# Kernel optimization log

Measured on AMD Instinct MI355X. Metric: run time of the kernel, lower is better.

The kernel has to match this reference:

```python
import jax, jax.numpy as jnp
import numpy as np

B, S, D = 2, 2048, 1024
H, KV, HD = 16, 4, 64
E, TOPK, F = 8, 2, 2048
EPS = 1e-5
THETA = 10000.0


def setup_inputs() -> dict:
    key = jax.random.key(0)
    ks = jax.random.split(key, 12)
    sc = 0.02
    x = jax.random.normal(ks[0], (B, S, D), jnp.float32)
    # real RoPE tables
    inv = 1.0 / (THETA ** (np.arange(0, HD, 2, dtype=np.float32) / HD))
    t = np.arange(S, dtype=np.float32)
    f = np.outer(t, inv)  # [S, HD/2]
    freqs_cos = jnp.asarray(np.cos(f), jnp.float32)
    freqs_sin = jnp.asarray(np.sin(f), jnp.float32)
    return {
        "x": x,
        "freqs_cos": freqs_cos,
        "freqs_sin": freqs_sin,
        "attn_norm_w": jnp.ones((D,), jnp.float32),
        "ffn_norm_w": jnp.ones((D,), jnp.float32),
        "wq": jax.random.normal(ks[1], (D, H * HD), jnp.float32) * sc,
        "wk": jax.random.normal(ks[2], (D, KV * HD), jnp.float32) * sc,
        "wv": jax.random.normal(ks[3], (D, KV * HD), jnp.float32) * sc,
        "wo": jax.random.normal(ks[4], (H * HD, D), jnp.float32) * sc,
        "gate_w": jax.random.normal(ks[5], (D, E), jnp.float32) * sc,
        "w1": jax.random.normal(ks[6], (E, D, F), jnp.float32) * sc,
        "w2": jax.random.normal(ks[7], (E, F, D), jnp.float32) * sc,
        "w3": jax.random.normal(ks[8], (E, D, F), jnp.float32) * sc,
    }


def rmsnorm(x, w):
    return x * jax.lax.rsqrt(jnp.mean(x * x, axis=-1, keepdims=True) + EPS) * w


def apply_rope(xq, cos, sin):
    # xq: [B,S,h,HD]; cos/sin: [S, HD/2]
    xr, xi = xq[..., 0::2], xq[..., 1::2]
    c = cos[None, :, None, :]
    s = sin[None, :, None, :]
    out = jnp.stack([xr * c - xi * s, xr * s + xi * c], axis=-1)
    return out.reshape(xq.shape)


def attention(xn, freqs_cos, freqs_sin, wq, wk, wv, wo):
    q = (xn @ wq).reshape(B, S, H, HD)
    k = (xn @ wk).reshape(B, S, KV, HD)
    v = (xn @ wv).reshape(B, S, KV, HD)
    q = apply_rope(q, freqs_cos, freqs_sin)
    k = apply_rope(k, freqs_cos, freqs_sin)
    n_rep = H // KV
    k = jnp.repeat(k, n_rep, axis=2)  # [B,S,H,HD]
    v = jnp.repeat(v, n_rep, axis=2)
    scores = jnp.einsum("bqhd,bkhd->bhqk", q, k) / jnp.sqrt(jnp.float32(HD))
    causal = jnp.tril(jnp.ones((S, S), bool))
    scores = jnp.where(causal[None, None], scores, jnp.finfo(scores.dtype).min)
    probs = jax.nn.softmax(scores, axis=-1)
    out = jnp.einsum("bhqk,bkhd->bqhd", probs, v).reshape(B, S, H * HD)
    return out @ wo


def sparse_moe(hn, gate_w, w1, w2, w3):
    xf = hn.reshape(-1, D)  # [T, D]
    probs = jax.nn.softmax(xf @ gate_w, axis=-1)  # [T, E]
    topv, topi = jax.lax.top_k(probs, TOPK)
    topv = topv / jnp.sum(topv, axis=-1, keepdims=True)
    # dense [T, E] routing weights (0 for non-selected experts)
    wdense = jnp.sum(jax.nn.one_hot(topi, E, dtype=xf.dtype) * topv[..., None], axis=1)
    h1 = jax.nn.silu(jnp.einsum("td,edf->etf", xf, w1))
    h3 = jnp.einsum("td,edf->etf", xf, w3)
    y = jnp.einsum("etf,efd->etd", h1 * h3, w2)
    out = jnp.einsum("te,etd->td", wdense, y)
    return out.reshape(B, S, D)


def reference(x, freqs_cos, freqs_sin, attn_norm_w, ffn_norm_w,
              wq, wk, wv, wo, gate_w, w1, w2, w3):
    h = x + attention(rmsnorm(x, attn_norm_w), freqs_cos, freqs_sin, wq, wk, wv, wo)
    out = h + sparse_moe(rmsnorm(h, ffn_norm_w), gate_w, w1, w2, w3)
    return out
```

## Files before the change

kernel.cpp:

```cpp
#include <hip/hip_runtime.h>
#include <stdint.h>

typedef unsigned short u16;
typedef unsigned int u32;
typedef __attribute__((ext_vector_type(8))) short short8;
typedef __attribute__((ext_vector_type(8))) u16 us8;
typedef __attribute__((ext_vector_type(4))) u16 us4;
typedef __attribute__((ext_vector_type(4))) float f32x4;

constexpr int NB = 2;
constexpr int SEQ = 2048;
constexpr int DIM = 1024;
constexpr int NH = 16;
constexpr int HD = 64;
constexpr int NE = 8;
constexpr int FF = 2048;
constexpr int TOK = NB * SEQ;
constexpr int NQKV = 1536;
constexpr int NPAIR = TOK * 2;
constexpr float REPS = 1e-5f;

__device__ __forceinline__ u16 f2bf(float x) {
  union { float f; u32 u; } v; v.f = x;
  u32 r = v.u + 0x7fffu + ((v.u >> 16) & 1u);
  return (u16)(r >> 16);
}
__device__ __forceinline__ float bf2f(u16 h) {
  union { u32 u; float f; } v; v.u = ((u32)h) << 16;
  return v.f;
}

template <bool SPLIT>
__global__ __launch_bounds__(256) void tcvt_k(const float* __restrict__ src,
                                              u16* __restrict__ dhi,
                                              u16* __restrict__ dlo,
                                              int K, int N) {
  int z = blockIdx.z;
  src += (size_t)z * K * N;
  dhi += (size_t)z * K * N;
  if (SPLIT) dlo += (size_t)z * K * N;
  int n0 = blockIdx.x * 64, k0 = blockIdx.y * 64;
  __shared__ float tile[64][65];
  int t = threadIdx.x;
  int kk = t >> 4, nn4 = (t & 15) * 4;
#pragma unroll
  for (int i = 0; i < 4; i++) {
    int k = kk + i * 16;
    const float* p = src + (size_t)(k0 + k) * N + n0 + nn4;
    float4 v = *(const float4*)p;
    tile[nn4 + 0][k] = v.x;
    tile[nn4 + 1][k] = v.y;
    tile[nn4 + 2][k] = v.z;
    tile[nn4 + 3][k] = v.w;
  }
  __syncthreads();
  int nn = t >> 4, k4 = (t & 15) * 4;
#pragma unroll
  for (int i = 0; i < 4; i++) {
    int n = nn + i * 16;
    us4 hi, lo;
#pragma unroll
    for (int j = 0; j < 4; j++) {
      float f = tile[n][k4 + j];
      u16 h = f2bf(f);
      hi[j] = h;
      if (SPLIT) lo[j] = f2bf(f - bf2f(h));
    }
    *(us4*)(dhi + (size_t)(n0 + n) * K + k0 + k4) = hi;
    if (SPLIT) *(us4*)(dlo + (size_t)(n0 + n) * K + k0 + k4) = lo;
  }
}

template <bool SPLIT>
__global__ __launch_bounds__(256) void rmsnorm_k(const float* __restrict__ x,
                                                 const float* __restrict__ w,
                                                 u16* __restrict__ ohi,
                                                 u16* __restrict__ olo) {
  int row = blockIdx.x, t = threadIdx.x;
  float4 v = *(const float4*)(x + (size_t)row * DIM + t * 4);
  float ss = v.x * v.x + v.y * v.y + v.z * v.z + v.w * v.w;
#pragma unroll
  for (int m = 1; m < 64; m <<= 1) ss += __shfl_xor(ss, m);
  __shared__ float red[4];
  if ((t & 63) == 0) red[t >> 6] = ss;
  __syncthreads();
  float rstd = rsqrtf((red[0] + red[1] + red[2] + red[3]) * (1.0f / DIM) + REPS);
  float4 wv = *(const float4*)(w + t * 4);
  float os[4] = {v.x * rstd * wv.x, v.y * rstd * wv.y, v.z * rstd * wv.z,
                 v.w * rstd * wv.w};
  us4 hi, lo;
#pragma unroll
  for (int j = 0; j < 4; j++) {
    u16 h = f2bf(os[j]);
    hi[j] = h;
    if (SPLIT) lo[j] = f2bf(os[j] - bf2f(h));
  }
  *(us4*)(ohi + (size_t)row * DIM + t * 4) = hi;
  if (SPLIT) *(us4*)(olo + (size_t)row * DIM + t * 4) = lo;
}

template <int EPI, bool SPLIT, bool GATHER, bool DUAL>
__global__ __launch_bounds__(256) void gemm_k(
    const u16* __restrict__ Ah, const u16* __restrict__ Al,
    const u16* __restrict__ Bh, const u16* __restrict__ Bl,
    const u16* __restrict__ B1, int M, int N, int K, int ldc,
    float* __restrict__ Cf, u16* __restrict__ Cb, float* __restrict__ C2,
    const float* __restrict__ resid, const int* __restrict__ cnt,
    const int* __restrict__ pids, const float* __restrict__ pw) {
  constexpr int BN = SPLIT ? 64 : 128;
  constexpr int WCOL = BN / 2;
  constexpr int FN = BN / 32;

  int z = blockIdx.z;
  {
    size_t boff = (size_t)z * N * K;
    Bh += boff;
    if (SPLIT) Bl += boff;
    if (DUAL) B1 += boff;
  }
  int m0 = blockIdx.y * 128, n0 = blockIdx.x * BN;
  int tid = threadIdx.x, lane = tid & 63, wid = tid >> 6;
  int wm = wid >> 1, wn = wid & 1;

  __shared__ u16 sAh[128 * 64];
  __shared__ u16 sAl[SPLIT ? 128 * 64 : 8];
  __shared__ u16 sBh[BN * 64];
  __shared__ u16 sBl[SPLIT ? BN * 64 : 8];
  __shared__ u16 sB1[DUAL ? BN * 64 : 8];
  __shared__ int spid[GATHER ? 128 : 8];
  __shared__ int srow[GATHER ? 128 : 8];

  int cntz = M;
  if (GATHER) {
    cntz = cnt[z];
    if (m0 >= cntz) return;
    if (tid < 128) {
      int i = m0 + tid;
      if (i > cntz - 1) i = cntz - 1;
      int p = pids[z * NPAIR + i];
      spid[tid] = p;
      srow[tid] = (EPI == 2) ? (p >> 1) : p;
    }
  }
  __syncthreads();

  f32x4 zv = {0.f, 0.f, 0.f, 0.f};
  f32x4 acc[4][FN];
  f32x4 acc1[4][FN];
#pragma unroll
  for (int a = 0; a < 4; a++)
#pragma unroll
    for (int b = 0; b < FN; b++) {
      acc[a][b] = zv;
      acc1[a][b] = zv;
    }

  for (int k0 = 0; k0 < K; k0 += 64) {
    __syncthreads();
#pragma unroll
    for (int i = 0; i < 4; i++) {
      int cid = tid + i * 256;
      int r = cid >> 3, c = cid & 7;
      int sw = r * 64 + ((c ^ (r & 7)) * 8);
      size_t ar = GATHER ? (size_t)srow[r] : (size_t)(m0 + r);
      *(us8*)&sAh[sw] = *(const us8*)(Ah + ar * K + k0 + c * 8);
      if (SPLIT) *(us8*)&sAl[sw] = *(const us8*)(Al + ar * K + k0 + c * 8);
    }
#pragma unroll
    for (int i = 0; i < FN; i++) {
      int cid = tid + i * 256;
      int r = cid >> 3, c = cid & 7;
      int sw = r * 64 + ((c ^ (r & 7)) * 8);
      size_t br = (size_t)(n0 + r) * K + k0 + c * 8;
      *(us8*)&sBh[sw] = *(const us8*)(Bh + br);
      if (SPLIT) *(us8*)&sBl[sw] = *(const us8*)(Bl + br);
      if (DUAL) *(us8*)&sB1[sw] = *(const us8*)(B1 + br);
    }
    __syncthreads();
#pragma unroll
    for (int kc = 0; kc < 2; kc++) {
      int rr = lane & 15;
      int sw = (((kc * 4 + (lane >> 4)) ^ (rr & 7)) * 8);
      short8 a_h[4], a_l[4], b_h[FN], b_l[FN], b1f[FN];
#pragma unroll
      for (int f = 0; f < 4; f++) {
        int ra = wm * 64 + f * 16 + rr;
        a_h[f] = *(const short8*)&sAh[ra * 64 + sw];
        if (SPLIT) a_l[f] = *(const short8*)&sAl[ra * 64 + sw];
      }
#pragma unroll
      for (int f = 0; f < FN; f++) {
        int rb = wn * WCOL + f * 16 + rr;
        b_h[f] = *(const short8*)&sBh[rb * 64 + sw];
        if (SPLIT) b_l[f] = *(const short8*)&sBl[rb * 64 + sw];
        if (DUAL) b1f[f] = *(const short8*)&sB1[rb * 64 + sw];
      }
#pragma unroll
      for (int fm = 0; fm < 4; fm++)
#pragma unroll
        for (int fn = 0; fn < FN; fn++) {
          acc[fm][fn] = __builtin_amdgcn_mfma_f32_16x16x32_bf16(
              a_h[fm], b_h[fn], acc[fm][fn], 0, 0, 0);
          if (SPLIT) {
            acc[fm][fn] = __builtin_amdgcn_mfma_f32_16x16x32_bf16(
                a_h[fm], b_l[fn], acc[fm][fn], 0, 0, 0);
            acc[fm][fn] = __builtin_amdgcn_mfma_f32_16x16x32_bf16(
                a_l[fm], b_h[fn], acc[fm][fn], 0, 0, 0);
          }
          if (DUAL)
            acc1[fm][fn] = __builtin_amdgcn_mfma_f32_16x16x32_bf16(
                a_h[fm], b1f[fn], acc1[fm][fn], 0, 0, 0);
        }
    }
  }

#pragma unroll
  for (int fm = 0; fm < 4; fm++)
#pragma unroll
    for (int fn = 0; fn < FN; fn++)
#pragma unroll
      for (int rg = 0; rg < 4; rg++) {
        int rl = wm * 64 + fm * 16 + (lane >> 4) * 4 + rg;
        int col = n0 + wn * WCOL + fn * 16 + (lane & 15);
        float v = acc[fm][fn][rg];
        if (EPI == 0) {
          Cf[(size_t)(m0 + rl) * ldc + col] = v;
        } else if (EPI == 1) {
          size_t idx = (size_t)(m0 + rl) * ldc + col;
          float r2 = v + resid[idx];
          Cf[idx] = r2;
          C2[idx] = r2;
        } else if (EPI == 2) {
          if (m0 + rl < cntz) {
            float g = v / (1.0f + __expf(-v));
            float o = g * acc1[fm][fn][rg];
            Cb[(size_t)spid[rl] * ldc + col] = f2bf(o);
          }
        } else {
          if (m0 + rl < cntz) {
            int p = spid[rl];
            atomicAdd(&Cf[(size_t)(p >> 1) * ldc + col], pw[p] * v);
          }
        }
      }
}

__global__ __launch_bounds__(256) void rope_k(float* __restrict__ qkv,
                                              const float* __restrict__ fc,
                                              const float* __restrict__ fs) {
  int idx = blockIdx.x * 256 + threadIdx.x;
  int i = idx & 31;
  int hh = (idx >> 5) % 20;
  int t = idx / 640;
  if (t >= TOK) return;
  int s = t & (SEQ - 1);
  int base = (hh < 16) ? (hh * 64) : (1024 + (hh - 16) * 64);
  float c = fc[s * 32 + i], sn = fs[s * 32 + i];
  float* p = qkv + (size_t)t * NQKV + base + 2 * i;
  float xr = p[0], xi = p[1];
  p[0] = xr * c - xi * sn;
  p[1] = xr * sn + xi * c;
}

__global__ __launch_bounds__(256) void cvtkv_k(const float* __restrict__ qkv,
                                               u16* __restrict__ Kh,
                                               u16* __restrict__ Kl,
                                               u16* __restrict__ Vh,
                                               u16* __restrict__ Vl) {
  int kvt = blockIdx.x;
  int kvh = blockIdx.y;
  int b = blockIdx.z;
  int t = threadIdx.x;
  __shared__ float vt[64][65];
  size_t tile = ((size_t)((b * 4 + kvh) * 32 + kvt)) * 4096;
  int r = t >> 2, c4 = t & 3;
  {
    const float* kp = qkv + ((size_t)(b * SEQ + kvt * 64 + r)) * NQKV + 1024 +
                      kvh * 64 + c4 * 16;
    float ff[16];
#pragma unroll
    for (int q = 0; q < 4; q++) {
      float4 f = *(const float4*)(kp + q * 4);
      ff[q * 4 + 0] = f.x; ff[q * 4 + 1] = f.y;
      ff[q * 4 + 2] = f.z; ff[q * 4 + 3] = f.w;
    }
#pragma unroll
    for (int half = 0; half < 2; half++) {
      int c = c4 * 2 + half;
      us8 hi, lo;
#pragma unroll
      for (int j = 0; j < 8; j++) {
        float f = ff[half * 8 + j];
        u16 h = f2bf(f);
        hi[j] = h;
        lo[j] = f2bf(f - bf2f(h));
      }
      int off = r * 64 + ((c ^ (r & 7)) * 8);
      *(us8*)(Kh + tile + off) = hi;
      *(us8*)(Kl + tile + off) = lo;
    }
  }
  {
    const float* vp = qkv + ((size_t)(b * SEQ + kvt * 64 + r)) * NQKV + 1280 +
                      kvh * 64 + c4 * 16;
#pragma unroll
    for (int q = 0; q < 4; q++) {
      float4 f = *(const float4*)(vp + q * 4);
      vt[r][c4 * 16 + q * 4 + 0] = f.x;
      vt[r][c4 * 16 + q * 4 + 1] = f.y;
      vt[r][c4 * 16 + q * 4 + 2] = f.z;
      vt[r][c4 * 16 + q * 4 + 3] = f.w;
    }
  }
  __syncthreads();
  {
    int d = t >> 2, g4 = t & 3;
    float ff[16];
#pragma unroll
    for (int j = 0; j < 16; j++) ff[j] = vt[g4 * 16 + j][d];
#pragma unroll
    for (int half = 0; half < 2; half++) {
      int c = g4 * 2 + half;
      us8 hi, lo;
#pragma unroll
      for (int j = 0; j < 8; j++) {
        float f = ff[half * 8 + j];
        u16 h = f2bf(f);
        hi[j] = h;
        lo[j] = f2bf(f - bf2f(h));
      }
      int off = d * 64 + ((c ^ (d & 7)) * 8);
      *(us8*)(Vh + tile + off) = hi;
      *(us8*)(Vl + tile + off) = lo;
    }
  }
}

__global__ __launch_bounds__(256, 2) void flash_k(
    const float* __restrict__ qkv, const u16* __restrict__ Kg,
    const u16* __restrict__ Klg, const u16* __restrict__ Vg,
    const u16* __restrict__ Vlg, u16* __restrict__ ah, u16* __restrict__ al) {
  int pi = blockIdx.x;
  int h = blockIdx.y;
  int b = blockIdx.z;
  int qt[2] = {31 - pi, pi};
  int kvh = h >> 2;
  int tid = threadIdx.x, lane = tid & 63, wid = tid >> 6;
  int rr = lane & 15, g = lane >> 4;

  __shared__ u16 sKh[4096], sKl[4096], sVh[4096], sVl[4096];
  __shared__ u32 sP[4][1024];

  f32x4 zv = {0.f, 0.f, 0.f, 0.f};
  short8 aqh[2][2], aql[2][2];
#pragma unroll
  for (int u = 0; u < 2; u++) {
    int qrow = qt[u] * 64 + wid * 16 + rr;
    const float* qp =
        qkv + ((size_t)(b * SEQ + qrow)) * NQKV + h * 64 + g * 8;
#pragma unroll
    for (int kc = 0; kc < 2; kc++) {
      float4 f0 = *(const float4*)(qp + kc * 32);
      float4 f1 = *(const float4*)(qp + kc * 32 + 4);
      float ff[8] = {f0.x, f0.y, f0.z, f0.w, f1.x, f1.y, f1.z, f1.w};
#pragma unroll
      for (int j = 0; j < 8; j++) {
        u16 hi = f2bf(ff[j]);
        aqh[u][kc][j] = (short)hi;
        aql[u][kc][j] = (short)f2bf(ff[j] - bf2f(hi));
      }
    }
  }

  f32x4 o[2][4];
  float m_r[2][4], l_r[2][4];
#pragma unroll
  for (int u = 0; u < 2; u++)
#pragma unroll
    for (int i = 0; i < 4; i++) {
      o[u][i] = zv;
      m_r[u][i] = -3.0e38f;
      l_r[u][i] = 0.f;
    }

  size_t tb = ((size_t)(b * 4 + kvh) * 32) * 4096;
  int so = tid * 16;
  us8 rKh[2], rKl[2], rVh[2], rVl[2];
  {
    size_t go = tb + so;
    rKh[0] = *(const us8*)(Kg + go);  rKh[1] = *(const us8*)(Kg + go + 8);
    rKl[0] = *(const us8*)(Klg + go); rKl[1] = *(const us8*)(Klg + go + 8);
    rVh[0] = *(const us8*)(Vg + go);  rVh[1] = *(const us8*)(Vg + go + 8);
    rVl[0] = *(const us8*)(Vlg + go); rVl[1] = *(const us8*)(Vlg + go + 8);
  }

  int nt = qt[0];
  for (int kvt = 0; kvt <= nt; kvt++) {
    __syncthreads();
    *(us8*)&sKh[so] = rKh[0]; *(us8*)&sKh[so + 8] = rKh[1];
    *(us8*)&sKl[so] = rKl[0]; *(us8*)&sKl[so + 8] = rKl[1];
    *(us8*)&sVh[so] = rVh[0]; *(us8*)&sVh[so + 8] = rVh[1];
    *(us8*)&sVl[so] = rVl[0]; *(us8*)&sVl[so + 8] = rVl[1];
    if (kvt < nt) {
      size_t go = tb + (size_t)(kvt + 1) * 4096 + so;
      rKh[0] = *(const us8*)(Kg + go);  rKh[1] = *(const us8*)(Kg + go + 8);
      rKl[0] = *(const us8*)(Klg + go); rKl[1] = *(const us8*)(Klg + go + 8);
      rVh[0] = *(const us8*)(Vg + go);  rVh[1] = *(const us8*)(Vg + go + 8);
      rVl[0] = *(const us8*)(Vlg + go); rVl[1] = *(const us8*)(Vlg + go + 8);
    }
    __syncthreads();

#pragma unroll
    for (int u = 0; u < 2; u++) {
      if (!(u == 1 && kvt > qt[1])) {
        float pv[4][4];
#pragma unroll
        for (int c16 = 0; c16 < 4; c16++) {
          int rk = c16 * 16 + rr;
          f32x4 sacc = zv;
#pragma unroll
          for (int kc = 0; kc < 2; kc++) {
            int sw = rk * 64 + (((kc * 4 + g) ^ (rk & 7)) * 8);
            short8 bh = *(const short8*)&sKh[sw];
            short8 bl = *(const short8*)&sKl[sw];
            sacc = __builtin_amdgcn_mfma_f32_16x16x32_bf16(aqh[u][kc], bh,
                                                           sacc, 0, 0, 0);
            sacc = __builtin_amdgcn_mfma_f32_16x16x32_bf16(aqh[u][kc], bl,
                                                           sacc, 0, 0, 0);
            sacc = __builtin_amdgcn_mfma_f32_16x16x32_bf16(aql[u][kc], bh,
                                                           sacc, 0, 0, 0);
          }
          bool diag = (kvt == qt[u]);
#pragma unroll
          for (int rg = 0; rg < 4; rg++) {
            float val = sacc[rg] * 0.125f;
            if (diag) {
              int kv_l = c16 * 16 + rr;
              int q_l = wid * 16 + g * 4 + rg;
              if (kv_l > q_l) val = -3.0e38f;
            }
            pv[c16][rg] = val;
          }
        }
        float pm[4];
#pragma unroll
        for (int rg = 0; rg < 4; rg++)
          pm[rg] = fmaxf(fmaxf(pv[0][rg], pv[1][rg]),
                         fmaxf(pv[2][rg], pv[3][rg]));
#pragma unroll
        for (int m = 1; m < 16; m <<= 1)
#pragma unroll
          for (int rg = 0; rg < 4; rg++)
            pm[rg] = fmaxf(pm[rg], __shfl_xor(pm[rg], m));
        float scl[4];
#pragma unroll
        for (int rg = 0; rg < 4; rg++) {
          float mn = fmaxf(m_r[u][rg], pm[rg]);
          scl[rg] = __expf(m_r[u][rg] - mn);
          m_r[u][rg] = mn;
        }
#pragma unroll
        for (int c16 = 0; c16 < 4; c16++)
#pragma unroll
          for (int rg = 0; rg < 4; rg++)
            pv[c16][rg] = __expf(pv[c16][rg] - m_r[u][rg]);
        float rsum[4];
#pragma unroll
        for (int rg = 0; rg < 4; rg++)
          rsum[rg] = pv[0][rg] + pv[1][rg] + pv[2][rg] + pv[3][rg];
#pragma unroll
        for (int m = 1; m < 16; m <<= 1)
#pragma unroll
          for (int rg = 0; rg < 4; rg++) rsum[rg] += __shfl_xor(rsum[rg], m);
#pragma unroll
        for (int rg = 0; rg < 4; rg++)
          l_r[u][rg] = l_r[u][rg] * scl[rg] + rsum[rg];
#pragma unroll
        for (int d16 = 0; d16 < 4; d16++)
#pragma unroll
          for (int rg = 0; rg < 4; rg++) o[u][d16][rg] *= scl[rg];

#pragma unroll
        for (int c16 = 0; c16 < 4; c16++)
#pragma unroll
          for (int rg = 0; rg < 4; rg++) {
            int ql = g * 4 + rg;
            int kvl = c16 * 16 + rr;
            u16 hi = f2bf(pv[c16][rg]);
            u16 lo = f2bf(pv[c16][rg] - bf2f(hi));
            sP[wid][ql * 64 + (kvl ^ (((ql >> 2) & 3) << 4))] =
                ((u32)lo << 16) | (u32)hi;
          }
        short8 pah[2], pal[2];
#pragma unroll
        for (int kc = 0; kc < 2; kc++) {
          int xb = (kc * 32 + g * 8) ^ (((rr >> 2) & 3) << 4);
          const u32* pp = &sP[wid][rr * 64 + xb];
#pragma unroll
          for (int j = 0; j < 8; j++) {
            u32 w = pp[j];
            pah[kc][j] = (short)(w & 0xffffu);
            pal[kc][j] = (short)(w >> 16);
          }
        }
#pragma unroll
        for (int d16 = 0; d16 < 4; d16++) {
          int rv = d16 * 16 + rr;
#pragma unroll
          for (int kc = 0; kc < 2; kc++) {
            int sw = rv * 64 + (((kc * 4 + g) ^ (rv & 7)) * 8);
            short8 vh = *(const short8*)&sVh[sw];
            short8 vl = *(const short8*)&sVl[sw];
            o[u][d16] = __builtin_amdgcn_mfma_f32_16x16x32_bf16(
                pah[kc], vh, o[u][d16], 0, 0, 0);
            o[u][d16] = __builtin_amdgcn_mfma_f32_16x16x32_bf16(
                pah[kc], vl, o[u][d16], 0, 0, 0);
            o[u][d16] = __builtin_amdgcn_mfma_f32_16x16x32_bf16(
                pal[kc], vh, o[u][d16], 0, 0, 0);
          }
        }
      }
    }
  }

#pragma unroll
  for (int u = 0; u < 2; u++)
#pragma unroll
    for (int rg = 0; rg < 4; rg++) {
      float inv = 1.0f / l_r[u][rg];
      int qr = qt[u] * 64 + wid * 16 + g * 4 + rg;
      size_t obase = (size_t)(b * SEQ + qr) * 1024 + h * 64;
#pragma unroll
      for (int d16 = 0; d16 < 4; d16++) {
        float v = o[u][d16][rg] * inv;
        u16 hi = f2bf(v);
        ah[obase + d16 * 16 + rr] = hi;
        al[obase + d16 * 16 + rr] = f2bf(v - bf2f(hi));
      }
    }
}

__global__ __launch_bounds__(256) void route_k(const float* __restrict__ h,
                                               const float* __restrict__ wffn,
                                               const float* __restrict__ gw,
                                               int* __restrict__ cnt,
                                               int* __restrict__ pids,
                                               float* __restrict__ pw) {
  int t = blockIdx.x, tid = threadIdx.x;
  float4 v = *(const float4*)(h + (size_t)t * DIM + tid * 4);
  float ss = v.x * v.x + v.y * v.y + v.z * v.z + v.w * v.w;
#pragma unroll
  for (int m = 1; m < 64; m <<= 1) ss += __shfl_xor(ss, m);
  __shared__ float red[4];
  if ((tid & 63) == 0) red[tid >> 6] = ss;
  __syncthreads();
  float rstd = rsqrtf((red[0] + red[1] + red[2] + red[3]) * (1.0f / DIM) + REPS);
  float4 wv = *(const float4*)(wffn + tid * 4);
  float xn[4] = {v.x * rstd * wv.x, v.y * rstd * wv.y, v.z * rstd * wv.z,
                 v.w * rstd * wv.w};
  float pl[8] = {0, 0, 0, 0, 0, 0, 0, 0};
#pragma unroll
  for (int j = 0; j < 4; j++) {
    const float* gp = gw + (size_t)(tid * 4 + j) * 8;
    float4 g0 = *(const float4*)gp;
    float4 g1 = *(const float4*)(gp + 4);
    pl[0] += xn[j] * g0.x; pl[1] += xn[j] * g0.y;
    pl[2] += xn[j] * g0.z; pl[3] += xn[j] * g0.w;
    pl[4] += xn[j] * g1.x; pl[5] += xn[j] * g1.y;
    pl[6] += xn[j] * g1.z; pl[7] += xn[j] * g1.w;
  }
#pragma unroll
  for (int e = 0; e < 8; e++)
#pragma unroll
    for (int m = 1; m < 64; m <<= 1) pl[e] += __shfl_xor(pl[e], m);
  __shared__ float lred[4][8];
  if ((tid & 63) == 0)
#pragma unroll
    for (int e = 0; e < 8; e++) lred[tid >> 6][e] = pl[e];
  __syncthreads();
  if (tid == 0) {
    float lg[8];
#pragma unroll
    for (int e = 0; e < 8; e++)
      lg[e] = lred[0][e] + lred[1][e] + lred[2][e] + lred[3][e];
    int e1 = 0;
    float l1 = lg[0];
#pragma unroll
    for (int e = 1; e < 8; e++)
      if (lg[e] > l1) { l1 = lg[e]; e1 = e; }
    int e2 = -1;
    float l2 = -3.0e38f;
#pragma unroll
    for (int e = 0; e < 8; e++)
      if (e != e1 && lg[e] > l2) { l2 = lg[e]; e2 = e; }
    float w1 = 1.0f / (1.0f + expf(l2 - l1));
    float w2 = 1.0f / (1.0f + expf(l1 - l2));
    int p0 = atomicAdd(&cnt[e1], 1);
    pids[e1 * NPAIR + p0] = t * 2;
    pw[t * 2] = w1;
    int p1 = atomicAdd(&cnt[e2], 1);
    pids[e2 * NPAIR + p1] = t * 2 + 1;
    pw[t * 2 + 1] = w2;
  }
}

__global__ void zero_k(int* cnt) {
  if (threadIdx.x < 8) cnt[threadIdx.x] = 0;
}

extern "C" void kernel_launch(void* const* d_in, const int* in_sizes, int n_in,
                              void* d_out, int out_size, void* d_ws,
                              size_t ws_size, hipStream_t stream) {
  (void)in_sizes; (void)n_in; (void)out_size; (void)ws_size;
  const float* x = (const float*)d_in[0];
  const float* fc = (const float*)d_in[1];
  const float* fs = (const float*)d_in[2];
  const float* anw = (const float*)d_in[3];
  const float* fnw = (const float*)d_in[4];
  const float* wq = (const float*)d_in[5];
  const float* wk = (const float*)d_in[6];
  const float* wv = (const float*)d_in[7];
  const float* wo = (const float*)d_in[8];
  const float* gw = (const float*)d_in[9];
  const float* w1 = (const float*)d_in[10];
  const float* w2 = (const float*)d_in[11];
  const float* w3 = (const float*)d_in[12];
  float* outf = (float*)d_out;

  char* ws = (char*)d_ws;
  size_t off = 0;
  auto alloc = [&](size_t bytes) {
    void* p = ws + off;
    off += (bytes + 255) & ~(size_t)255;
    return p;
  };
  u16* wqkvT_h = (u16*)alloc((size_t)NQKV * DIM * 2);
  u16* wqkvT_l = (u16*)alloc((size_t)NQKV * DIM * 2);
  u16* woT_h = (u16*)alloc((size_t)DIM * DIM * 2);
  u16* woT_l = (u16*)alloc((size_t)DIM * DIM * 2);
  u16* w1T = (u16*)alloc((size_t)NE * FF * DIM * 2);
  u16* w3T = (u16*)alloc((size_t)NE * FF * DIM * 2);
  u16* w2T = (u16*)alloc((size_t)NE * DIM * FF * 2);
  u16* xnh = (u16*)alloc((size_t)TOK * DIM * 2);
  u16* xnl = (u16*)alloc((size_t)TOK * DIM * 2);
  float* qkvf = (float*)alloc((size_t)TOK * NQKV * 4);
  u16* attnh = (u16*)alloc((size_t)TOK * DIM * 2);
  u16* attnl = (u16*)alloc((size_t)TOK * DIM * 2);
  float* hbuf = (float*)alloc((size_t)TOK * DIM * 4);
  u16* hn = (u16*)alloc((size_t)TOK * DIM * 2);
  u16* h13 = (u16*)alloc((size_t)NPAIR * FF * 2);
  int* cnt = (int*)alloc(32);
  int* pids = (int*)alloc((size_t)NE * NPAIR * 4);
  float* pwbuf = (float*)alloc((size_t)NPAIR * 4);
  u16* Ksw_h = (u16*)alloc((size_t)NB * 4 * SEQ * 64 * 2);
  u16* Ksw_l = (u16*)alloc((size_t)NB * 4 * SEQ * 64 * 2);
  u16* Vsw_h = (u16*)alloc((size_t)NB * 4 * SEQ * 64 * 2);
  u16* Vsw_l = (u16*)alloc((size_t)NB * 4 * SEQ * 64 * 2);

  dim3 blk(256);
  hipLaunchKernelGGL((tcvt_k<true>), dim3(16, 16, 1), blk, 0, stream, wq,
                     wqkvT_h, wqkvT_l, 1024, 1024);
  hipLaunchKernelGGL((tcvt_k<true>), dim3(4, 16, 1), blk, 0, stream, wk,
                     wqkvT_h + 1024 * 1024, wqkvT_l + 1024 * 1024, 1024, 256);
  hipLaunchKernelGGL((tcvt_k<true>), dim3(4, 16, 1), blk, 0, stream, wv,
                     wqkvT_h + 1280 * 1024, wqkvT_l + 1280 * 1024, 1024, 256);
  hipLaunchKernelGGL((tcvt_k<true>), dim3(16, 16, 1), blk, 0, stream, wo, woT_h,
                     woT_l, 1024, 1024);
  hipLaunchKernelGGL((tcvt_k<false>), dim3(32, 16, 8), blk, 0, stream, w1, w1T,
                     (u16*)nullptr, 1024, 2048);
  hipLaunchKernelGGL((tcvt_k<false>), dim3(32, 16, 8), blk, 0, stream, w3, w3T,
                     (u16*)nullptr, 1024, 2048);
  hipLaunchKernelGGL((tcvt_k<false>), dim3(16, 32, 8), blk, 0, stream, w2, w2T,
                     (u16*)nullptr, 2048, 1024);
  hipLaunchKernelGGL((rmsnorm_k<true>), dim3(TOK), blk, 0, stream, x, anw, xnh,
                     xnl);
  hipLaunchKernelGGL((gemm_k<0, true, false, false>),
                     dim3(NQKV / 64, TOK / 128, 1), blk, 0, stream, xnh, xnl,
                     wqkvT_h, wqkvT_l, (const u16*)nullptr, TOK, NQKV, DIM,
                     NQKV, qkvf, (u16*)nullptr, (float*)nullptr,
                     (const float*)nullptr, (const int*)nullptr,
                     (const int*)nullptr, (const float*)nullptr);
  hipLaunchKernelGGL(rope_k, dim3((TOK * 20 * 32) / 256), blk, 0, stream, qkvf,
                     fc, fs);
  hipLaunchKernelGGL(cvtkv_k, dim3(SEQ / 64, 4, NB), blk, 0, stream, qkvf,
                     Ksw_h, Ksw_l, Vsw_h, Vsw_l);
  hipLaunchKernelGGL(flash_k, dim3(16, NH, NB), blk, 0, stream, qkvf, Ksw_h,
                     Ksw_l, Vsw_h, Vsw_l, attnh, attnl);
  hipLaunchKernelGGL((gemm_k<1, true, false, false>),
                     dim3(DIM / 64, TOK / 128, 1), blk, 0, stream, attnh, attnl,
                     woT_h, woT_l, (const u16*)nullptr, TOK, DIM, DIM, DIM,
                     hbuf, (u16*)nullptr, outf, x, (const int*)nullptr,
                     (const int*)nullptr, (const float*)nullptr);
  hipLaunchKernelGGL((rmsnorm_k<false>), dim3(TOK), blk, 0, stream, hbuf, fnw,
                     hn, (u16*)nullptr);
  hipLaunchKernelGGL(zero_k, dim3(1), dim3(64), 0, stream, cnt);
  hipLaunchKernelGGL(route_k, dim3(TOK), blk, 0, stream, hbuf, fnw, gw, cnt,
                     pids, pwbuf);
  hipLaunchKernelGGL((gemm_k<2, false, true, true>),
                     dim3(FF / 128, NPAIR / 128, NE), blk, 0, stream, hn,
                     (const u16*)nullptr, w1T, (const u16*)nullptr, w3T, NPAIR,
                     FF, DIM, FF, (float*)nullptr, h13, (float*)nullptr,
                     (const float*)nullptr, cnt, pids, pwbuf);
  hipLaunchKernelGGL((gemm_k<3, false, true, false>),
                     dim3(DIM / 128, NPAIR / 128, NE), blk, 0, stream, h13,
                     (const u16*)nullptr, w2T, (const u16*)nullptr,
                     (const u16*)nullptr, NPAIR, DIM, FF, DIM, outf,
                     (u16*)nullptr, (float*)nullptr, (const float*)nullptr, cnt,
                     pids, pwbuf);
}
```

Baseline: 651.0 us.

## Pipeline GEMM with triple-buffered direct-to-LDS loads and persistent MoE scheduling

```diff
diff --git a/kernel.cpp b/kernel.cpp
--- a/kernel.cpp
+++ b/kernel.cpp
@@ -20,6 +20,9 @@
 constexpr int NPAIR = TOK * 2;
 constexpr float REPS = 1e-5f;
 
+#define VMCNT(n) asm volatile("s_waitcnt vmcnt(" #n ")" ::: "memory")
+#define LGKM0 asm volatile("s_waitcnt lgkmcnt(0)" ::: "memory")
+
 __device__ __forceinline__ u16 f2bf(float x) {
   union { float f; u32 u; } v; v.f = x;
   u32 r = v.u + 0x7fffu + ((v.u >> 16) & 1u);
@@ -28,6 +31,12 @@
 __device__ __forceinline__ float bf2f(u16 h) {
   union { u32 u; float f; } v; v.u = ((u32)h) << 16;
   return v.f;
+}
+
+__device__ __forceinline__ void gl_lds16(const u16* g, u16* l) {
+  __builtin_amdgcn_global_load_lds(
+      (const __attribute__((address_space(1))) void*)g,
+      (__attribute__((address_space(3))) void*)l, 16, 0, 0);
 }
 
 template <bool SPLIT>
@@ -99,101 +108,170 @@
   if (SPLIT) *(us4*)(olo + (size_t)row * DIM + t * 4) = lo;
 }
 
-template <int EPI, bool SPLIT, bool GATHER, bool DUAL>
-__global__ __launch_bounds__(256) void gemm_k(
+template <int EPI, bool SPLIT, bool DUAL, bool PERSIST, int NXL, int NT>
+__global__ __launch_bounds__(256, 2) void gemm_k(
     const u16* __restrict__ Ah, const u16* __restrict__ Al,
     const u16* __restrict__ Bh, const u16* __restrict__ Bl,
-    const u16* __restrict__ B1, int M, int N, int K, int ldc,
+    const u16* __restrict__ B1, int N, int ldc,
     float* __restrict__ Cf, u16* __restrict__ Cb, float* __restrict__ C2,
     const float* __restrict__ resid, const int* __restrict__ cnt,
-    const int* __restrict__ pids, const float* __restrict__ pw) {
+    const int* __restrict__ pids, const float* __restrict__ pw,
+    const int* __restrict__ plan) {
+  constexpr int K = NT * 32;
   constexpr int BN = SPLIT ? 64 : 128;
   constexpr int WCOL = BN / 2;
   constexpr int FN = BN / 32;
-
-  int z = blockIdx.z;
-  {
-    size_t boff = (size_t)z * N * K;
-    Bh += boff;
-    if (SPLIT) Bl += boff;
-    if (DUAL) B1 += boff;
-  }
-  int m0 = blockIdx.y * 128, n0 = blockIdx.x * BN;
+  constexpr int NAI = 2;
+  constexpr int NBI = BN / 64;
+  constexpr int BUFA = 128 * 32;
+  constexpr int BUFB = BN * 32;
+  constexpr bool L6 = SPLIT || DUAL;
+
   int tid = threadIdx.x, lane = tid & 63, wid = tid >> 6;
   int wm = wid >> 1, wn = wid & 1;
-
-  __shared__ u16 sAh[128 * 64];
-  __shared__ u16 sAl[SPLIT ? 128 * 64 : 8];
-  __shared__ u16 sBh[BN * 64];
-  __shared__ u16 sBl[SPLIT ? BN * 64 : 8];
-  __shared__ u16 sB1[DUAL ? BN * 64 : 8];
-  __shared__ int spid[GATHER ? 128 : 8];
-  __shared__ int srow[GATHER ? 128 : 8];
-
-  int cntz = M;
-  if (GATHER) {
-    cntz = cnt[z];
-    if (m0 >= cntz) return;
-    if (tid < 128) {
-      int i = m0 + tid;
-      if (i > cntz - 1) i = cntz - 1;
-      int p = pids[z * NPAIR + i];
-      spid[tid] = p;
-      srow[tid] = (EPI == 2) ? (p >> 1) : p;
-    }
-  }
-  __syncthreads();
-
-  f32x4 zv = {0.f, 0.f, 0.f, 0.f};
-  f32x4 acc[4][FN];
-  f32x4 acc1[4][FN];
-#pragma unroll
-  for (int a = 0; a < 4; a++)
-#pragma unroll
-    for (int b = 0; b < FN; b++) {
-      acc[a][b] = zv;
-      acc1[a][b] = zv;
-    }
-
-  for (int k0 = 0; k0 < K; k0 += 64) {
-    __syncthreads();
-#pragma unroll
-    for (int i = 0; i < 4; i++) {
-      int cid = tid + i * 256;
-      int r = cid >> 3, c = cid & 7;
-      int sw = r * 64 + ((c ^ (r & 7)) * 8);
-      size_t ar = GATHER ? (size_t)srow[r] : (size_t)(m0 + r);
-      *(us8*)&sAh[sw] = *(const us8*)(Ah + ar * K + k0 + c * 8);
-      if (SPLIT) *(us8*)&sAl[sw] = *(const us8*)(Al + ar * K + k0 + c * 8);
-    }
-#pragma unroll
-    for (int i = 0; i < FN; i++) {
-      int cid = tid + i * 256;
-      int r = cid >> 3, c = cid & 7;
-      int sw = r * 64 + ((c ^ (r & 7)) * 8);
-      size_t br = (size_t)(n0 + r) * K + k0 + c * 8;
-      *(us8*)&sBh[sw] = *(const us8*)(Bh + br);
-      if (SPLIT) *(us8*)&sBl[sw] = *(const us8*)(Bl + br);
-      if (DUAL) *(us8*)&sB1[sw] = *(const us8*)(B1 + br);
-    }
-    __syncthreads();
-#pragma unroll
-    for (int kc = 0; kc < 2; kc++) {
-      int rr = lane & 15;
-      int sw = (((kc * 4 + (lane >> 4)) ^ (rr & 7)) * 8);
+  int rr = lane & 15, g = lane >> 4;
+
+  __shared__ u16 sAh[3 * BUFA];
+  __shared__ u16 sAl[SPLIT ? 3 * BUFA : 16];
+  __shared__ u16 sBh[3 * BUFB];
+  __shared__ u16 sBl[SPLIT ? 3 * BUFB : 16];
+  __shared__ u16 sB1[DUAL ? 3 * BUFB : 16];
+  __shared__ int spid[PERSIST ? 128 : 8];
+  __shared__ int srow[PERSIST ? 128 : 8];
+
+  int pl[9];
+  int items;
+  if (PERSIST) {
+#pragma unroll
+    for (int e = 0; e < 9; e++) pl[e] = plan[e];
+    items = pl[8] << NXL;
+  } else {
+    items = 1;
+  }
+
+  int it0 = PERSIST ? blockIdx.x : 0;
+  int itstep = PERSIST ? gridDim.x : 1;
+  for (int w = it0; w < items; w += itstep) {
+    int m0, n0, z, cntz;
+    if (PERSIST) {
+      int wy = w >> NXL;
+      int x = w & ((1 << NXL) - 1);
+      z = 0;
+#pragma unroll
+      for (int e = 1; e < 8; e++) z += (wy >= pl[e]) ? 1 : 0;
+      int yt = wy - pl[z];
+      m0 = yt * 128;
+      n0 = x * BN;
+      cntz = cnt[z];
+      if (tid < 128) {
+        int i = m0 + tid;
+        if (i > cntz - 1) i = cntz - 1;
+        int p = pids[z * NPAIR + i];
+        spid[tid] = p;
+        srow[tid] = (EPI == 2) ? (p >> 1) : p;
+      }
+      __syncthreads();
+    } else {
+      m0 = blockIdx.y * 128;
+      n0 = blockIdx.x * BN;
+      z = 0;
+      cntz = 1 << 30;
+    }
+
+    const u16* Bhz = Bh + (size_t)z * N * K;
+    const u16* Blz = SPLIT ? Bl + (size_t)z * N * K : nullptr;
+    const u16* B1z = DUAL ? B1 + (size_t)z * N * K : nullptr;
+
+    int p4 = lane & 3;
+    const u16 *agh[NAI], *agl[NAI];
+    int aoff[NAI];
+#pragma unroll
+    for (int i = 0; i < NAI; i++) {
+      int rl = i * 64 + wid * 16 + (lane >> 2);
+      int gr = PERSIST ? srow[rl] : (m0 + rl);
+      int sc = p4 ^ (rl & 3);
+      agh[i] = Ah + (size_t)gr * K + sc * 8;
+      if (SPLIT) agl[i] = Al + (size_t)gr * K + sc * 8;
+      aoff[i] = (i * 4 + wid) * 512;
+    }
+    const u16 *bgh[NBI], *bgl[NBI], *bg1[NBI];
+    int boff[NBI];
+#pragma unroll
+    for (int i = 0; i < NBI; i++) {
+      int rl = i * 64 + wid * 16 + (lane >> 2);
+      int sc = p4 ^ (rl & 3);
+      size_t gr = (size_t)(n0 + rl) * K + sc * 8;
+      bgh[i] = Bhz + gr;
+      if (SPLIT) bgl[i] = Blz + gr;
+      if (DUAL) bg1[i] = B1z + gr;
+      boff[i] = (i * 4 + wid) * 512;
+    }
+
+    auto STAGE = [&](int kt, int bi) {
+      int k0 = kt * 32;
+#pragma unroll
+      for (int i = 0; i < NAI; i++) {
+        gl_lds16(agh[i] + k0, sAh + bi * BUFA + aoff[i]);
+        if (SPLIT) gl_lds16(agl[i] + k0, sAl + bi * BUFA + aoff[i]);
+      }
+#pragma unroll
+      for (int i = 0; i < NBI; i++) {
+        gl_lds16(bgh[i] + k0, sBh + bi * BUFB + boff[i]);
+        if (SPLIT) gl_lds16(bgl[i] + k0, sBl + bi * BUFB + boff[i]);
+        if (DUAL) gl_lds16(bg1[i] + k0, sB1 + bi * BUFB + boff[i]);
+      }
+    };
+
+    f32x4 zv = {0.f, 0.f, 0.f, 0.f};
+    f32x4 acc[4][FN];
+    f32x4 acc1[DUAL ? 4 : 1][DUAL ? FN : 1];
+#pragma unroll
+    for (int a = 0; a < 4; a++)
+#pragma unroll
+      for (int b = 0; b < FN; b++) {
+        acc[a][b] = zv;
+        if (DUAL) acc1[a][b] = zv;
+      }
+
+    STAGE(0, 0);
+    STAGE(1, 1);
+    STAGE(2, 2);
+
+    int bi = 0;
+    for (int t = 0; t < NT; t++) {
+      int og = NT - 1 - t;
+      if (L6) {
+        if (og >= 2) VMCNT(12);
+        else if (og == 1) VMCNT(6);
+        else VMCNT(0);
+      } else {
+        if (og >= 2) VMCNT(8);
+        else if (og == 1) VMCNT(4);
+        else VMCNT(0);
+      }
+      __builtin_amdgcn_s_barrier();
+
+      const u16* bA = sAh + bi * BUFA;
+      const u16* bAl = sAl + (SPLIT ? bi * BUFA : 0);
+      const u16* bB = sBh + bi * BUFB;
+      const u16* bBl = sBl + (SPLIT ? bi * BUFB : 0);
+      const u16* bB1 = sB1 + (DUAL ? bi * BUFB : 0);
+
       short8 a_h[4], a_l[4], b_h[FN], b_l[FN], b1f[FN];
 #pragma unroll
       for (int f = 0; f < 4; f++) {
         int ra = wm * 64 + f * 16 + rr;
-        a_h[f] = *(const short8*)&sAh[ra * 64 + sw];
-        if (SPLIT) a_l[f] = *(const short8*)&sAl[ra * 64 + sw];
+        int off = ra * 32 + ((g ^ (ra & 3)) * 8);
+        a_h[f] = *(const short8*)&bA[off];
+        if (SPLIT) a_l[f] = *(const short8*)&bAl[off];
       }
 #pragma unroll
       for (int f = 0; f < FN; f++) {
         int rb = wn * WCOL + f * 16 + rr;
-        b_h[f] = *(const short8*)&sBh[rb * 64 + sw];
-        if (SPLIT) b_l[f] = *(const short8*)&sBl[rb * 64 + sw];
-        if (DUAL) b1f[f] = *(const short8*)&sB1[rb * 64 + sw];
+        int off = rb * 32 + ((g ^ (rb & 3)) * 8);
+        b_h[f] = *(const short8*)&bB[off];
+        if (SPLIT) b_l[f] = *(const short8*)&bBl[off];
+        if (DUAL) b1f[f] = *(const short8*)&bB1[off];
       }
 #pragma unroll
       for (int fm = 0; fm < 4; fm++)
@@ -211,38 +289,44 @@
             acc1[fm][fn] = __builtin_amdgcn_mfma_f32_16x16x32_bf16(
                 a_h[fm], b1f[fn], acc1[fm][fn], 0, 0, 0);
         }
-    }
-  }
-
-#pragma unroll
-  for (int fm = 0; fm < 4; fm++)
-#pragma unroll
-    for (int fn = 0; fn < FN; fn++)
-#pragma unroll
-      for (int rg = 0; rg < 4; rg++) {
-        int rl = wm * 64 + fm * 16 + (lane >> 4) * 4 + rg;
-        int col = n0 + wn * WCOL + fn * 16 + (lane & 15);
-        float v = acc[fm][fn][rg];
-        if (EPI == 0) {
-          Cf[(size_t)(m0 + rl) * ldc + col] = v;
-        } else if (EPI == 1) {
-          size_t idx = (size_t)(m0 + rl) * ldc + col;
-          float r2 = v + resid[idx];
-          Cf[idx] = r2;
-          C2[idx] = r2;
-        } else if (EPI == 2) {
-          if (m0 + rl < cntz) {
-            float g = v / (1.0f + __expf(-v));
-            float o = g * acc1[fm][fn][rg];
-            Cb[(size_t)spid[rl] * ldc + col] = f2bf(o);
-          }
-        } else {
-          if (m0 + rl < cntz) {
-            int p = spid[rl];
-            atomicAdd(&Cf[(size_t)(p >> 1) * ldc + col], pw[p] * v);
+
+      LGKM0;
+      __builtin_amdgcn_s_barrier();
+      if (t + 3 < NT) STAGE(t + 3, bi);
+      bi = (bi == 2) ? 0 : bi + 1;
+    }
+
+#pragma unroll
+    for (int fm = 0; fm < 4; fm++)
+#pragma unroll
+      for (int fn = 0; fn < FN; fn++)
+#pragma unroll
+        for (int rg = 0; rg < 4; rg++) {
+          int rl = wm * 64 + fm * 16 + g * 4 + rg;
+          int col = n0 + wn * WCOL + fn * 16 + rr;
+          float v = acc[fm][fn][rg];
+          if (EPI == 0) {
+            Cf[(size_t)(m0 + rl) * ldc + col] = v;
+          } else if (EPI == 1) {
+            size_t idx = (size_t)(m0 + rl) * ldc + col;
+            float r2 = v + resid[idx];
+            Cf[idx] = r2;
+            C2[idx] = r2;
+          } else if (EPI == 2) {
+            if (m0 + rl < cntz) {
+              float gg = v / (1.0f + __expf(-v));
+              float o = gg * acc1[fm][fn][rg];
+              Cb[(size_t)spid[rl] * ldc + col] = f2bf(o);
+            }
+          } else {
+            if (m0 + rl < cntz) {
+              int p = spid[rl];
+              atomicAdd(&Cf[(size_t)(p >> 1) * ldc + col], pw[p] * v);
+            }
           }
         }
-      }
+    if (PERSIST) __syncthreads();
+  }
 }
 
 __global__ __launch_bounds__(256) void rope_k(float* __restrict__ qkv,
@@ -606,6 +690,17 @@
 
 __global__ void zero_k(int* cnt) {
   if (threadIdx.x < 8) cnt[threadIdx.x] = 0;
+}
+
+__global__ void plan_k(const int* __restrict__ cnt, int* __restrict__ plan) {
+  if (threadIdx.x == 0) {
+    int acc = 0;
+    for (int e = 0; e < 8; e++) {
+      plan[e] = acc;
+      acc += (cnt[e] + 127) >> 7;
+    }
+    plan[8] = acc;
+  }
 }
 
 extern "C" void kernel_launch(void* const* d_in, const int* in_sizes, int n_in,
@@ -649,7 +744,8 @@
   float* hbuf = (float*)alloc((size_t)TOK * DIM * 4);
   u16* hn = (u16*)alloc((size_t)TOK * DIM * 2);
   u16* h13 = (u16*)alloc((size_t)NPAIR * FF * 2);
-  int* cnt = (int*)alloc(32);
+  int* cnt = (int*)alloc(64);
+  int* plan = (int*)alloc(64);
   int* pids = (int*)alloc((size_t)NE * NPAIR * 4);
   float* pwbuf = (float*)alloc((size_t)NPAIR * 4);
   u16* Ksw_h = (u16*)alloc((size_t)NB * 4 * SEQ * 64 * 2);
@@ -674,37 +770,37 @@
                      (u16*)nullptr, 2048, 1024);
   hipLaunchKernelGGL((rmsnorm_k<true>), dim3(TOK), blk, 0, stream, x, anw, xnh,
                      xnl);
-  hipLaunchKernelGGL((gemm_k<0, true, false, false>),
+  hipLaunchKernelGGL((gemm_k<0, true, false, false, 0, 32>),
                      dim3(NQKV / 64, TOK / 128, 1), blk, 0, stream, xnh, xnl,
-                     wqkvT_h, wqkvT_l, (const u16*)nullptr, TOK, NQKV, DIM,
-                     NQKV, qkvf, (u16*)nullptr, (float*)nullptr,
-                     (const float*)nullptr, (const int*)nullptr,
-                     (const int*)nullptr, (const float*)nullptr);
+                     wqkvT_h, wqkvT_l, (const u16*)nullptr, NQKV, NQKV, qkvf,
+                     (u16*)nullptr, (float*)nullptr, (const float*)nullptr,
+                     (const int*)nullptr, (const int*)nullptr,
+                     (const float*)nullptr, (const int*)nullptr);
   hipLaunchKernelGGL(rope_k, dim3((TOK * 20 * 32) / 256), blk, 0, stream, qkvf,
                      fc, fs);
   hipLaunchKernelGGL(cvtkv_k, dim3(SEQ / 64, 4, NB), blk, 0, stream, qkvf,
                      Ksw_h, Ksw_l, Vsw_h, Vsw_l);
   hipLaunchKernelGGL(flash_k, dim3(16, NH, NB), blk, 0, stream, qkvf, Ksw_h,
                      Ksw_l, Vsw_h, Vsw_l, attnh, attnl);
-  hipLaunchKernelGGL((gemm_k<1, true, false, false>),
+  hipLaunchKernelGGL((gemm_k<1, true, false, false, 0, 32>),
                      dim3(DIM / 64, TOK / 128, 1), blk, 0, stream, attnh, attnl,
-                     woT_h, woT_l, (const u16*)nullptr, TOK, DIM, DIM, DIM,
-                     hbuf, (u16*)nullptr, outf, x, (const int*)nullptr,
-                     (const int*)nullptr, (const float*)nullptr);
+                     woT_h, woT_l, (const u16*)nullptr, DIM, DIM, hbuf,
+                     (u16*)nullptr, outf, x, (const int*)nullptr,
+                     (const int*)nullptr, (const float*)nullptr,
+                     (const int*)nullptr);
   hipLaunchKernelGGL((rmsnorm_k<false>), dim3(TOK), blk, 0, stream, hbuf, fnw,
                      hn, (u16*)nullptr);
   hipLaunchKernelGGL(zero_k, dim3(1), dim3(64), 0, stream, cnt);
   hipLaunchKernelGGL(route_k, dim3(TOK), blk, 0, stream, hbuf, fnw, gw, cnt,
                      pids, pwbuf);
-  hipLaunchKernelGGL((gemm_k<2, false, true, true>),
-                     dim3(FF / 128, NPAIR / 128, NE), blk, 0, stream, hn,
-                     (const u16*)nullptr, w1T, (const u16*)nullptr, w3T, NPAIR,
-                     FF, DIM, FF, (float*)nullptr, h13, (float*)nullptr,
-                     (const float*)nullptr, cnt, pids, pwbuf);
-  hipLaunchKernelGGL((gemm_k<3, false, true, false>),
-                     dim3(DIM / 128, NPAIR / 128, NE), blk, 0, stream, h13,
-                     (const u16*)nullptr, w2T, (const u16*)nullptr,
-                     (const u16*)nullptr, NPAIR, DIM, FF, DIM, outf,
-                     (u16*)nullptr, (float*)nullptr, (const float*)nullptr, cnt,
-                     pids, pwbuf);
-}
+  hipLaunchKernelGGL(plan_k, dim3(1), dim3(64), 0, stream, cnt, plan);
+  hipLaunchKernelGGL((gemm_k<2, false, true, true, 4, 32>), dim3(1024), blk, 0,
+                     stream, hn, (const u16*)nullptr, w1T, (const u16*)nullptr,
+                     w3T, FF, FF, (float*)nullptr, h13, (float*)nullptr,
+                     (const float*)nullptr, cnt, pids, pwbuf, plan);
+  hipLaunchKernelGGL((gemm_k<3, false, false, true, 3, 64>), dim3(1024), blk, 0,
+                     stream, h13, (const u16*)nullptr, w2T, (const u16*)nullptr,
+                     (const u16*)nullptr, DIM, DIM, outf, (u16*)nullptr,
+                     (float*)nullptr, (const float*)nullptr, cnt, pids, pwbuf,
+                     plan);
+}
```

Result: faster. 626.8 us (-3.7%).
